# Optimization experiments

Hardware: AMD Instinct MI355X
Metric: run time of the kernel (lower is better)

Reference implementation:

```python
import jax, jax.numpy as jnp
import numpy as np

K = 8      # neighbors (from __init__ default k=8)
EPS = 1e-5 # BatchNorm1d default eps


def conv1x1(x, w, b):
    # x: (B,C,N), w: (O,C), b: (O,) -> (B,O,N)
    return jnp.einsum('bcn,oc->bon', x, w) + b[None, :, None]


def batchnorm(x, g, be):
    # training-mode BatchNorm1d: stats over (B, N) per channel
    m = x.mean(axis=(0, 2), keepdims=True)
    v = x.var(axis=(0, 2), keepdims=True)
    return g[None, :, None] * (x - m) * jax.lax.rsqrt(v + EPS) + be[None, :, None]


def block(x, w, b, g, be):
    return jax.nn.relu(batchnorm(conv1x1(x, w, b), g, be))


def setup_inputs() -> dict:
    key = jax.random.key(0)
    ks = jax.random.split(key, 24)
    B, N = 16, 4096
    rn = lambda k, s, sc=0.1: jax.random.normal(k, s, jnp.float32) * sc
    ones_n = lambda k, s: jnp.ones(s, jnp.float32) + rn(k, s, 0.01)
    return {
        'points': jax.random.normal(ks[0], (B, N, 3), jnp.float32),
        'w1': rn(ks[1], (64, 3)),   'b1': rn(ks[2], (64,)),
        'g1': ones_n(ks[3], (64,)), 'be1': rn(ks[4], (64,)),
        'w3': rn(ks[5], (512, 64)), 'b3': rn(ks[6], (512,)),
        'g3': ones_n(ks[7], (512,)), 'be3': rn(ks[8], (512,)),
        'hw1': rn(ks[9], (512, 1088)), 'hb1': rn(ks[10], (512,)),
        'hg1': ones_n(ks[11], (512,)), 'hbe1': rn(ks[12], (512,)),
        'hw2': rn(ks[13], (256, 512)), 'hb2': rn(ks[14], (256,)),
        'hg2': ones_n(ks[15], (256,)), 'hbe2': rn(ks[16], (256,)),
        'hw3': rn(ks[17], (128, 256)), 'hb3': rn(ks[18], (128,)),
        'hg3': ones_n(ks[19], (128,)), 'hbe3': rn(ks[20], (128,)),
        'hw4': rn(ks[21], (6, 128)), 'hb4': rn(ks[22], (6,)),
    }


def reference(points, w1, b1, g1, be1, w3, b3, g3, be3,
              hw1, hb1, hg1, hbe1, hw2, hb2, hg2, hbe2,
              hw3, hb3, hg3, hbe3, hw4, hb4):
    B, N, _ = points.shape
    # brute-force KNN (squared L2, ascending -> top_k on -dist)
    x2 = jnp.sum(points * points, axis=-1)                     # (B,N)
    dist = x2[:, :, None] + x2[:, None, :] \
        - 2.0 * jnp.einsum('bnd,bmd->bnm', points, points)      # (B,N,N)
    idx = jax.lax.top_k(-dist, K)[1]                           # (B,N,K) int32

    p = points.transpose(0, 2, 1)                              # (B,3,N)
    l_feat = block(p, w1, b1, g1, be1)                         # (B,64,N)
    x = block(l_feat, w3, b3, g3, be3)                         # (B,512,N)
    x_t = x.transpose(0, 2, 1)                                 # (B,N,512)

    # Faithful to the original's gather bug:
    # out[b,n,k,c] = x_t[b, idx[b,n,k], k]  (independent of c since K<512)
    vals = jnp.take_along_axis(x_t[:, :, :K], idx, axis=1)     # (B,N,K)
    m = vals.max(axis=2)                                       # (B,N)
    local_features = jnp.broadcast_to(m[:, None, :], (B, 512, N))

    global_feat = jnp.broadcast_to(x.max(axis=2, keepdims=True), (B, 512, N))
    h = jnp.concatenate([local_features, l_feat, global_feat], axis=1)  # (B,1088,N)
    h = block(h, hw1, hb1, hg1, hbe1)
    h = block(h, hw2, hb2, hg2, hbe2)
    h = block(h, hw3, hb3, hg3, hbe3)
    h = conv1x1(h, hw4, hb4)                                   # (B,6,N)
    return h.transpose(0, 2, 1)                                # (B,N,6)
```

## Files before the change

### kernel.cpp

```cpp
#include <hip/hip_runtime.h>
#include <hip/hip_bf16.h>
#include <math.h>

typedef __attribute__((ext_vector_type(8))) short short8;
typedef __attribute__((ext_vector_type(16))) float f32x16;

__device__ inline f32x16 mfma32(short8 a, short8 b, f32x16 c) {
    return __builtin_amdgcn_mfma_f32_32x32x16_bf16(a, b, c, 0, 0, 0);
}

__device__ inline void bsplit(float x, ushort& h, ushort& l) {
    __hip_bfloat16 bh = __float2bfloat16(x);
    float hf = __bfloat162float(bh);
    __hip_bfloat16 bl = __float2bfloat16(x - hf);
    h = *reinterpret_cast<ushort*>(&bh);
    l = *reinterpret_cast<ushort*>(&bl);
}

__device__ inline float unmap_f(unsigned int mp) {
    unsigned int db = mp ^ (0x80000000u | (unsigned int)((int)(~mp) >> 31));
    return __uint_as_float(db);
}

__global__ void k_wsplit_all(
    const float* __restrict__ w3s, const float* __restrict__ hw1,
    const float* __restrict__ hw2, const float* __restrict__ hw3,
    const float* __restrict__ hw4,
    ushort* __restrict__ w3h, ushort* __restrict__ w3l,
    ushort* __restrict__ w1eh, ushort* __restrict__ w1el,
    ushort* __restrict__ w2h, ushort* __restrict__ w2l,
    ushort* __restrict__ wh3h, ushort* __restrict__ wh3l,
    ushort* __restrict__ w4h, ushort* __restrict__ w4l) {
    int i = blockIdx.x * 256 + threadIdx.x;
    const float* src; int rs, co, Ms, K, base; ushort *hi, *lo;
    if (i < 32768)       { src = w3s; rs = 64;   co = 0;   Ms = 512; K = 64;  hi = w3h;  lo = w3l;  base = 0; }
    else if (i < 65536)  { src = hw1; rs = 1088; co = 512; Ms = 512; K = 64;  hi = w1eh; lo = w1el; base = 32768; }
    else if (i < 196608) { src = hw2; rs = 512;  co = 0;   Ms = 256; K = 512; hi = w2h;  lo = w2l;  base = 65536; }
    else if (i < 229376) { src = hw3; rs = 256;  co = 0;   Ms = 128; K = 256; hi = wh3h; lo = wh3l; base = 196608; }
    else if (i < 233472) { src = hw4; rs = 128;  co = 0;   Ms = 6;   K = 128; hi = w4h;  lo = w4l;  base = 229376; }
    else return;
    int li = i - base;
    int o = li / K, k = li - o * K;
    float x = (o < Ms) ? src[(size_t)o * rs + co + k] : 0.f;
    ushort h, l;
    bsplit(x, h, l);
    hi[li] = h; lo[li] = l;
}

__global__ void k_stats1(const float* __restrict__ pts, const float* __restrict__ w1,
                         const float* __restrict__ b1, float* __restrict__ part1) {
    __shared__ float sw[256];
    __shared__ float wred[2][4][64];
    int t = threadIdx.x;
    if (t < 192) sw[t] = w1[t];
    if (t < 64) sw[192 + t] = b1[t];
    __syncthreads();
    int g = blockIdx.x * 256 + t;
    float p0 = pts[g*3], p1 = pts[g*3+1], p2 = pts[g*3+2];
    int lane = t & 63, wv = t >> 6;
    for (int c = 0; c < 64; c++) {
        float y = fmaf(sw[c*3+2], p2, fmaf(sw[c*3+1], p1, fmaf(sw[c*3], p0, sw[192+c])));
        float s = y, q = y * y;
        #pragma unroll
        for (int o = 32; o > 0; o >>= 1) { s += __shfl_down(s, o); q += __shfl_down(q, o); }
        if (lane == 0) { wred[0][wv][c] = s; wred[1][wv][c] = q; }
    }
    __syncthreads();
    if (t < 64) {
        float s = wred[0][0][t] + wred[0][1][t] + wred[0][2][t] + wred[0][3][t];
        float q = wred[1][0][t] + wred[1][1][t] + wred[1][2][t] + wred[1][3][t];
        part1[blockIdx.x * 128 + t] = s;
        part1[blockIdx.x * 128 + 64 + t] = q;
    }
}

__global__ void k_fin(const float* __restrict__ part, int count, int stride, int sqoff,
                      const float* __restrict__ g, const float* __restrict__ be,
                      float* __restrict__ sout, float* __restrict__ tout) {
    int c = blockIdx.x, t = threadIdx.x;
    float s = 0.f, q = 0.f;
    for (int w = t; w < count; w += 256) { s += part[(size_t)w*stride + c]; q += part[(size_t)w*stride + sqoff + c]; }
    __shared__ float rs[4], rq[4];
    int lane = t & 63, wv = t >> 6;
    #pragma unroll
    for (int o = 32; o > 0; o >>= 1) { s += __shfl_down(s, o); q += __shfl_down(q, o); }
    if (lane == 0) { rs[wv] = s; rq[wv] = q; }
    __syncthreads();
    if (t == 0) {
        s = rs[0] + rs[1] + rs[2] + rs[3];
        q = rq[0] + rq[1] + rq[2] + rq[3];
        float mean = s / 65536.f;
        float var = q / 65536.f - mean * mean;
        float sc = g[c] * rsqrtf(var + 1e-5f);
        sout[c] = sc;
        tout[c] = be[c] - mean * sc;
    }
}

__global__ void k_lfeat2(const float* __restrict__ pts, const float* __restrict__ w1,
                         const float* __restrict__ b1, const float* __restrict__ s1,
                         const float* __restrict__ t1, ushort* __restrict__ lfh,
                         ushort* __restrict__ lfl) {
    __shared__ float sw[256], ss[64], st[64];
    int t = threadIdx.x;
    if (t < 192) sw[t] = w1[t];
    if (t < 64) { sw[192+t] = b1[t]; ss[t] = s1[t]; st[t] = t1[t]; }
    __syncthreads();
    int g = blockIdx.x * 256 + t;
    float p0 = pts[g*3], p1 = pts[g*3+1], p2 = pts[g*3+2];
    for (int c0 = 0; c0 < 64; c0 += 8) {
        union { short8 v; ushort u[8]; } H, L;
        #pragma unroll
        for (int j = 0; j < 8; j++) {
            int c = c0 + j;
            float y = fmaf(sw[c*3+2], p2, fmaf(sw[c*3+1], p1, fmaf(sw[c*3], p0, sw[192+c])));
            float a = fmaxf(fmaf(ss[c], y, st[c]), 0.f);
            bsplit(a, H.u[j], L.u[j]);
        }
        *(short8*)(lfh + (size_t)g*64 + c0) = H.v;
        *(short8*)(lfl + (size_t)g*64 + c0) = L.v;
    }
}

template<int MODE>
__global__ __launch_bounds__(256, 2) void k_gemm64(
    const ushort* __restrict__ Bhi, const ushort* __restrict__ Blo,
    const ushort* __restrict__ Ahi, const ushort* __restrict__ Alo,
    const float* __restrict__ bias, const float* __restrict__ A1,
    const float* __restrict__ G1, const float* __restrict__ mb,
    float* __restrict__ part, float* __restrict__ y38) {
    __shared__ ushort sbh[128*64], sbl[128*64];
    __shared__ float sPb[512], sPa[512];
    int t = threadIdx.x, pb = blockIdx.x;
    int gn0 = pb * 128, b = pb >> 5;
    for (int i = t; i < 512; i += 256) {
        float bb = bias[i];
        if (MODE) bb += G1[(b<<9) + i];
        sPb[i] = bb;
        sPa[i] = MODE ? A1[i] : 0.f;
    }
    for (int it = 0; it < 4; it++) {
        int s = it*256 + t;
        int n = s >> 3, c16 = s & 7;
        int off = (c16*16) ^ ((n & 7) << 4);
        int sb8 = (it*256 + (t & 192)) * 8;
        __builtin_amdgcn_global_load_lds((const char*)Bhi + (size_t)(gn0+n)*128 + off, &sbh[sb8], 16, 0, 0);
        __builtin_amdgcn_global_load_lds((const char*)Blo + (size_t)(gn0+n)*128 + off, &sbl[sb8], 16, 0, 0);
    }
    __syncthreads();
    int lane = t & 63, wv = t >> 6, m = lane & 31, kg = lane >> 5;
    for (int ct = 0; ct < 4; ct++) {
        int ch0 = wv*128 + ct*32;
        short8 ah[4], al[4];
        #pragma unroll
        for (int ks = 0; ks < 4; ks++) {
            ah[ks] = *(const short8*)(Ahi + (size_t)(ch0+m)*64 + ks*16 + kg*8);
            al[ks] = *(const short8*)(Alo + (size_t)(ch0+m)*64 + ks*16 + kg*8);
        }
        float ssum[16] = {}, ssq[16] = {}, smx[16];
        #pragma unroll
        for (int r = 0; r < 16; r++) smx[r] = -__builtin_inff();
        for (int pt = 0; pt < 4; pt++) {
            int n = pt*32 + m;
            f32x16 acc = {};
            #pragma unroll
            for (int ks = 0; ks < 4; ks++) {
                int off = ((ks*16 + kg*8)*2) ^ ((n & 7) << 4);
                short8 bh = *(const short8*)((const char*)sbh + n*128 + off);
                short8 bl = *(const short8*)((const char*)sbl + n*128 + off);
                acc = mfma32(ah[ks], bh, acc);
                acc = mfma32(ah[ks], bl, acc);
                acc = mfma32(al[ks], bh, acc);
            }
            float mval = MODE ? mb[gn0 + n] : 0.f;
            #pragma unroll
            for (int r = 0; r < 16; r++) {
                int chr = ch0 + (r&3) + 8*(r>>2) + 4*kg;
                float v = acc[r] + sPb[chr] + (MODE ? sPa[chr]*mval : 0.f);
                ssum[r] += v; ssq[r] = fmaf(v, v, ssq[r]);
                if (MODE == 0) {
                    smx[r] = fmaxf(smx[r], v);
                    if (wv == 0 && ct == 0 && r < 4) {
                        int c8 = (r&3) + 4*kg;
                        y38[(size_t)c8*65536 + gn0 + n] = v;
                    }
                }
            }
        }
        #pragma unroll
        for (int r = 0; r < 16; r++) {
            float s = ssum[r], q = ssq[r], x = smx[r];
            #pragma unroll
            for (int o = 16; o > 0; o >>= 1) {
                s += __shfl_xor(s, o); q += __shfl_xor(q, o);
                if (MODE == 0) x = fmaxf(x, __shfl_xor(x, o));
            }
            if (m == 0) {
                int chr = ch0 + (r&3) + 8*(r>>2) + 4*kg;
                if (MODE == 0) {
                    part[(size_t)pb*1536 + chr] = s;
                    part[(size_t)pb*1536 + 512 + chr] = q;
                    part[(size_t)pb*1536 + 1024 + chr] = x;
                } else {
                    part[(size_t)pb*1024 + chr] = s;
                    part[(size_t)pb*1024 + 512 + chr] = q;
                }
            }
        }
    }
}

__global__ void k_fin3b(const float* __restrict__ part3, const float* __restrict__ s3,
                        const float* __restrict__ t3, float* __restrict__ gmaxb) {
    int b = blockIdx.x, c = threadIdx.x;
    float mx = -__builtin_inff();
    for (int i = 0; i < 32; i++) mx = fmaxf(mx, part3[(size_t)(b*32+i)*1536 + 1024 + c]);
    gmaxb[(b<<9)+c] = fmaxf(fmaf(s3[c], mx, t3[c]), 0.f);
}

__global__ void k_a1g1(const float* __restrict__ hw1, const float* __restrict__ gmaxb,
                       float* __restrict__ A1, float* __restrict__ G1) {
    __shared__ float sg[512];
    int blk = blockIdx.x, t = threadIdx.x;
    if (blk < 32) {
        int b = blk >> 1;
        for (int i = t; i < 512; i += 256) sg[i] = gmaxb[(b<<9)+i];
        __syncthreads();
        int o = (blk & 1)*256 + t;
        float s = 0.f;
        for (int c4 = 0; c4 < 128; c4++) {
            float4 w = *(const float4*)&hw1[(size_t)o*1088 + 576 + c4*4];
            s = fmaf(w.x, sg[c4*4],   s);
            s = fmaf(w.y, sg[c4*4+1], s);
            s = fmaf(w.z, sg[c4*4+2], s);
            s = fmaf(w.w, sg[c4*4+3], s);
        }
        G1[(b<<9)+o] = s;
    } else {
        int o = (blk - 32)*256 + t;
        float s = 0.f;
        for (int c4 = 0; c4 < 128; c4++) {
            float4 w = *(const float4*)&hw1[(size_t)o*1088 + c4*4];
            s += w.x; s += w.y; s += w.z; s += w.w;
        }
        A1[o] = s;
    }
}

__global__ __launch_bounds__(1024, 8)
void k_knn(const float* __restrict__ pts, const float* __restrict__ y38,
           const float* __restrict__ s3, const float* __restrict__ t3,
           float* __restrict__ mbuf) {
    __shared__ float4 sp[4096];
    int t = threadIdx.x, blk = blockIdx.x;
    int b = blk >> 5;
    int lane = t & 63, wv = t >> 6;
    const float* pb = pts + (size_t)b * 4096 * 3;
    for (int i = t; i < 4096; i += 1024) {
        float c0 = pb[i*3], c1 = pb[i*3+1], c2 = pb[i*3+2];
        float cw = __fadd_rn(__fadd_rn(__fmul_rn(c0,c0), __fmul_rn(c1,c1)), __fmul_rn(c2,c2));
        sp[i] = make_float4(c0, c1, c2, cw);
    }
    __syncthreads();
    const int NINF = 0xff800000;
    int qbase = (blk & 31) * 128 + wv * 8;
    for (int pass = 0; pass < 2; ++pass) {
        int qb = qbase + pass*4;
        float q0[4], q1[4], q2[4], qx2[4];
        #pragma unroll
        for (int qi = 0; qi < 4; qi++) {
            float4 qp = sp[qb + qi];
            q0[qi] = qp.x; q1[qi] = qp.y; q2[qi] = qp.z; qx2[qi] = qp.w;
        }
        float sd[4]; unsigned int si[4]; float thr[4];
        {
            float4 cp = sp[lane];
            #pragma unroll
            for (int qi = 0; qi < 4; qi++) {
                float dot = __fadd_rn(__fadd_rn(__fmul_rn(q0[qi],cp.x), __fmul_rn(q1[qi],cp.y)), __fmul_rn(q2[qi],cp.z));
                float d = __fsub_rn(__fadd_rn(qx2[qi], cp.w), __fmul_rn(2.f, dot));
                unsigned int db = __float_as_uint(d);
                unsigned int mp = db ^ (0x80000000u | (unsigned int)((int)db >> 31));
                unsigned long long key = ((unsigned long long)mp << 32) | (unsigned int)lane;
                #pragma unroll
                for (int k = 2; k <= 64; k <<= 1) {
                    #pragma unroll
                    for (int jj = k >> 1; jj >= 1; jj >>= 1) {
                        unsigned long long pk = __shfl_xor(key, jj);
                        bool up = ((lane & k) == 0);
                        bool lower = ((lane & jj) == 0);
                        bool keepmin = (lower == up);
                        unsigned long long mn = (pk < key) ? pk : key;
                        unsigned long long mx = (pk < key) ? key : pk;
                        key = keepmin ? mn : mx;
                    }
                }
                sd[qi] = unmap_f((unsigned int)(key >> 32));
                si[qi] = (unsigned int)key;
                thr[qi] = __shfl(sd[qi], 7);
            }
        }
        for (int j = 1; j < 64; j++) {
            float4 cp = sp[j*64 + lane];
            #pragma unroll
            for (int qi = 0; qi < 4; qi++) {
                float dot = __fadd_rn(__fadd_rn(__fmul_rn(q0[qi],cp.x), __fmul_rn(q1[qi],cp.y)), __fmul_rn(q2[qi],cp.z));
                float d = __fsub_rn(__fadd_rn(qx2[qi], cp.w), __fmul_rn(2.f, dot));
                unsigned long long mask = __ballot(d < thr[qi]);
                if (mask != 0ull) {
                    do {
                        int src = __ffsll(mask) - 1;
                        float db = __uint_as_float(__builtin_amdgcn_readlane(__float_as_uint(d), src));
                        unsigned int mb_ = (unsigned int)(j*64 + src);
                        float pd = __int_as_float(__builtin_amdgcn_update_dpp(
                            NINF, __float_as_int(sd[qi]), 0x111, 0xf, 0xf, false));
                        unsigned int pi = (unsigned int)__builtin_amdgcn_update_dpp(
                            0, (int)si[qi], 0x111, 0xf, 0xf, false);
                        bool keep = (sd[qi] <= db);
                        bool pk = (pd <= db);
                        sd[qi] = keep ? sd[qi] : (pk ? db : pd);
                        si[qi] = keep ? si[qi] : (pk ? mb_ : pi);
                        mask &= (mask - 1ull);
                    } while (mask != 0ull);
                    thr[qi] = __shfl(sd[qi], 7);
                }
            }
        }
        if (lane < 8) {
            #pragma unroll
            for (int qi = 0; qi < 4; qi++) {
                float y = y38[(size_t)lane*65536 + (b<<12) + (si[qi] & 4095)];
                float mv = fmaxf(fmaf(s3[lane], y, t3[lane]), 0.f);
                mv = fmaxf(mv, __shfl_xor(mv, 1));
                mv = fmaxf(mv, __shfl_xor(mv, 2));
                mv = fmaxf(mv, __shfl_xor(mv, 4));
                if (lane == 0) mbuf[(b<<12) + qb + qi] = mv;
            }
        }
    }
}

__global__ __launch_bounds__(256, 2) void k_h2f(
    const ushort* __restrict__ lfh, const ushort* __restrict__ lfl,
    const ushort* __restrict__ W1hi, const ushort* __restrict__ W1lo,
    const ushort* __restrict__ W2hi, const ushort* __restrict__ W2lo,
    const float* __restrict__ hb1, const float* __restrict__ A1g,
    const float* __restrict__ G1g, const float* __restrict__ mb,
    const float* __restrict__ sh1, const float* __restrict__ th1,
    const float* __restrict__ hb2,
    float* __restrict__ pre2, float* __restrict__ parth2) {
    __shared__ ushort sLh[128*64], sLl[128*64];
    __shared__ ushort a1h[128*64], a1l[128*64];
    __shared__ float sP0[512], sP1[512], sSh[512];
    int t = threadIdx.x, pb = blockIdx.x;
    int gn0 = pb * 128, b = pb >> 5;
    for (int i = t; i < 512; i += 256) {
        float s = sh1[i];
        sP0[i] = fmaf(s, hb1[i] + G1g[(b<<9)+i], th1[i]);
        sP1[i] = s * A1g[i];
        sSh[i] = s;
    }
    for (int it = 0; it < 4; it++) {
        int s = it*256 + t;
        int n = s >> 3, c16 = s & 7;
        int off = (c16*16) ^ ((n & 7) << 4);
        int sb8 = (it*256 + (t & 192)) * 8;
        __builtin_amdgcn_global_load_lds((const char*)lfh + (size_t)(gn0+n)*128 + off, &sLh[sb8], 16, 0, 0);
        __builtin_amdgcn_global_load_lds((const char*)lfl + (size_t)(gn0+n)*128 + off, &sLl[sb8], 16, 0, 0);
    }
    __syncthreads();
    int lane = t & 63, wv = t >> 6, m = lane & 31, kg = lane >> 5;
    int pn = wv*32 + m;
    float mval = mb[gn0 + pn];
    f32x16 acc0[4] = {}, acc1[4] = {};
    for (int ch = 0; ch < 8; ch++) {
        #pragma unroll
        for (int cht = 0; cht < 2; cht++) {
            int cch = ch*64 + cht*32;
            f32x16 acc = {};
            #pragma unroll
            for (int ks = 0; ks < 4; ks++) {
                short8 ah = *(const short8*)(W1hi + (size_t)(cch+m)*64 + ks*16 + kg*8);
                short8 al = *(const short8*)(W1lo + (size_t)(cch+m)*64 + ks*16 + kg*8);
                int off = ((ks*16 + kg*8)*2) ^ ((m & 7) << 4);
                short8 bh = *(const short8*)((const char*)sLh + pn*128 + off);
                short8 bl = *(const short8*)((const char*)sLl + pn*128 + off);
                acc = mfma32(ah, bh, acc);
                acc = mfma32(ah, bl, acc);
                acc = mfma32(al, bh, acc);
            }
            #pragma unroll
            for (int q = 0; q < 4; q++) {
                ushort hs[4], ls[4];
                #pragma unroll
                for (int i = 0; i < 4; i++) {
                    int r = q*4 + i;
                    int chr = cch + i + 8*q + 4*kg;
                    float a = fmaxf(fmaf(sSh[chr], acc[r], sP0[chr] + sP1[chr]*mval), 0.f);
                    bsplit(a, hs[i], ls[i]);
                }
                int chb = cht*32 + 8*q + 4*kg;
                int off = (chb*2) ^ ((m & 7) << 4);
                uint2 vh, vl;
                vh.x = (uint)hs[0] | ((uint)hs[1] << 16); vh.y = (uint)hs[2] | ((uint)hs[3] << 16);
                vl.x = (uint)ls[0] | ((uint)ls[1] << 16); vl.y = (uint)ls[2] | ((uint)ls[3] << 16);
                *(uint2*)((char*)a1h + pn*128 + off) = vh;
                *(uint2*)((char*)a1l + pn*128 + off) = vl;
            }
        }
        __syncthreads();
        #pragma unroll
        for (int ks = 0; ks < 4; ks++) {
            int koc = ks*16 + kg*8;
            int kglob = ch*64 + koc;
            short8 w0h = *(const short8*)(W2hi + (size_t)(wv*64+m)*512 + kglob);
            short8 w0l = *(const short8*)(W2lo + (size_t)(wv*64+m)*512 + kglob);
            short8 w1h = *(const short8*)(W2hi + (size_t)(wv*64+32+m)*512 + kglob);
            short8 w1l = *(const short8*)(W2lo + (size_t)(wv*64+32+m)*512 + kglob);
            #pragma unroll
            for (int pt = 0; pt < 4; pt++) {
                int n = pt*32 + m;
                int off = (koc*2) ^ ((n & 7) << 4);
                short8 bh = *(const short8*)((const char*)a1h + n*128 + off);
                short8 bl = *(const short8*)((const char*)a1l + n*128 + off);
                acc0[pt] = mfma32(w0h, bh, acc0[pt]);
                acc1[pt] = mfma32(w1h, bh, acc1[pt]);
                acc0[pt] = mfma32(w0h, bl, acc0[pt]);
                acc1[pt] = mfma32(w1h, bl, acc1[pt]);
                acc0[pt] = mfma32(w0l, bh, acc0[pt]);
                acc1[pt] = mfma32(w1l, bh, acc1[pt]);
            }
        }
        __syncthreads();
    }
    #pragma unroll
    for (int ti = 0; ti < 2; ti++) {
        #pragma unroll
        for (int r = 0; r < 16; r++) {
            int chr = wv*64 + ti*32 + (r&3) + 8*(r>>2) + 4*kg;
            float hb = hb2[chr];
            float s = 0.f, q = 0.f;
            #pragma unroll
            for (int pt = 0; pt < 4; pt++) {
                float v = (ti ? acc1[pt][r] : acc0[pt][r]) + hb;
                pre2[(size_t)chr*65536 + gn0 + pt*32 + m] = v;
                s += v; q = fmaf(v, v, q);
            }
            #pragma unroll
            for (int o = 16; o > 0; o >>= 1) { s += __shfl_xor(s, o); q += __shfl_xor(q, o); }
            if (m == 0) {
                parth2[(size_t)pb*512 + chr] = s;
                parth2[(size_t)pb*512 + 256 + chr] = q;
            }
        }
    }
}

__global__ __launch_bounds__(256, 2) void k_h3s(
    const float* __restrict__ pre2, const float* __restrict__ sh2,
    const float* __restrict__ th2,
    const ushort* __restrict__ W3hi, const ushort* __restrict__ W3lo,
    const float* __restrict__ hb3, float* __restrict__ parth3,
    float* __restrict__ pre3) {
    __shared__ ushort sbh[32*256], sbl[32*256];
    __shared__ float ft[128*36];
    __shared__ float sS2[256], sT2[256];
    int t = threadIdx.x, pb = blockIdx.x;
    sS2[t] = sh2[t]; sT2[t] = th2[t];
    int lane = t & 63, wv = t >> 6, m = lane & 31, kg = lane >> 5;
    int ch0 = wv * 32;
    int cn = t & 31, cgq = t >> 5;
    float bhr[16];
    #pragma unroll
    for (int r = 0; r < 16; r++) bhr[r] = hb3[ch0 + (r&3) + 8*(r>>2) + 4*kg];
    float ssum[16] = {}, ssq[16] = {};
    for (int pt = 0; pt < 4; pt++) {
        int gn0 = pb*128 + pt*32;
        for (int h = 0; h < 2; h++) {
            __syncthreads();
            #pragma unroll
            for (int i = 0; i < 4; i++) {
                int idx = i*256 + t;
                int row = idx >> 3, c4 = idx & 7;
                float4 v = *(const float4*)(pre2 + (size_t)(h*128+row)*65536 + gn0 + c4*4);
                float* dst = &ft[row*36 + c4*4];
                dst[0] = v.x; dst[1] = v.y; dst[2] = v.z; dst[3] = v.w;
            }
            __syncthreads();
            #pragma unroll
            for (int i4 = 0; i4 < 4; i4++) {
                int cl0 = cgq*16 + i4*4;
                int cg0 = h*128 + cl0;
                ushort hs[4], ls[4];
                #pragma unroll
                for (int i = 0; i < 4; i++) {
                    float v = fmaxf(fmaf(sS2[cg0+i], ft[(cl0+i)*36 + cn], sT2[cg0+i]), 0.f);
                    bsplit(v, hs[i], ls[i]);
                }
                int off = cn*512 + (((cg0 >> 3)*16) ^ ((cn & 15) << 4)) + (cg0 & 7)*2;
                uint2 vh, vl;
                vh.x = (uint)hs[0] | ((uint)hs[1] << 16); vh.y = (uint)hs[2] | ((uint)hs[3] << 16);
                vl.x = (uint)ls[0] | ((uint)ls[1] << 16); vl.y = (uint)ls[2] | ((uint)ls[3] << 16);
                *(uint2*)((char*)sbh + off) = vh;
                *(uint2*)((char*)sbl + off) = vl;
            }
        }
        __syncthreads();
        f32x16 acc = {};
        for (int ks = 0; ks < 16; ks++) {
            int ko = ks*16 + kg*8;
            int off = (ko*2) ^ ((m & 15) << 4);
            short8 bh = *(const short8*)((const char*)sbh + m*512 + off);
            short8 bl = *(const short8*)((const char*)sbl + m*512 + off);
            short8 ah = *(const short8*)(W3hi + (size_t)(ch0+m)*256 + ko);
            short8 al = *(const short8*)(W3lo + (size_t)(ch0+m)*256 + ko);
            acc = mfma32(ah, bh, acc);
            acc = mfma32(ah, bl, acc);
            acc = mfma32(al, bh, acc);
        }
        #pragma unroll
        for (int r = 0; r < 16; r++) {
            float v = acc[r] + bhr[r];
            int chr = ch0 + (r&3) + 8*(r>>2) + 4*kg;
            pre3[(size_t)chr*65536 + gn0 + m] = v;
            ssum[r] += v; ssq[r] = fmaf(v, v, ssq[r]);
        }
    }
    #pragma unroll
    for (int r = 0; r < 16; r++) {
        float s = ssum[r], q = ssq[r];
        #pragma unroll
        for (int o = 16; o > 0; o >>= 1) { s += __shfl_xor(s, o); q += __shfl_xor(q, o); }
        if (m == 0) {
            int chr = ch0 + (r&3) + 8*(r>>2) + 4*kg;
            parth3[(size_t)pb*256 + chr] = s;
            parth3[(size_t)pb*256 + 128 + chr] = q;
        }
    }
}

__global__ __launch_bounds__(256) void k_h4l(
    const float* __restrict__ pre3, const float* __restrict__ sh3,
    const float* __restrict__ th3, const float* __restrict__ hw4,
    const float* __restrict__ hb4, float* __restrict__ out) {
    __shared__ float a3[128*66];
    __shared__ float sW[6*128];
    __shared__ float sB[8];
    int t = threadIdx.x, pb = blockIdx.x;
    int n0 = pb * 64;
    for (int i = t; i < 768; i += 256) sW[i] = hw4[i];
    if (t < 6) sB[t] = hb4[t];
    #pragma unroll
    for (int k = 0; k < 32; k++) {
        int i = k*256 + t;
        int c = i >> 6, col = i & 63;
        float v = pre3[(size_t)c*65536 + n0 + col];
        a3[c*66 + col] = fmaxf(fmaf(sh3[c], v, th3[c]), 0.f);
    }
    __syncthreads();
    int p = t & 63, grp = t >> 6;
    if (grp < 3) {
        float a0 = sB[grp*2], a1 = sB[grp*2+1];
        const float* w0 = &sW[(grp*2)*128];
        const float* w1 = &sW[(grp*2+1)*128];
        #pragma unroll 4
        for (int c = 0; c < 128; c++) {
            float x = a3[c*66 + p];
            a0 = fmaf(w0[c], x, a0);
            a1 = fmaf(w1[c], x, a1);
        }
        out[(size_t)(n0+p)*6 + grp*2]     = a0;
        out[(size_t)(n0+p)*6 + grp*2 + 1] = a1;
    }
}

extern "C" void kernel_launch(void* const* d_in, const int* in_sizes, int n_in,
                              void* d_out, int out_size, void* d_ws, size_t ws_size,
                              hipStream_t stream) {
    const float* pts  = (const float*)d_in[0];
    const float* w1   = (const float*)d_in[1];
    const float* b1   = (const float*)d_in[2];
    const float* g1   = (const float*)d_in[3];
    const float* be1  = (const float*)d_in[4];
    const float* w3   = (const float*)d_in[5];
    const float* b3   = (const float*)d_in[6];
    const float* g3   = (const float*)d_in[7];
    const float* be3  = (const float*)d_in[8];
    const float* hw1  = (const float*)d_in[9];
    const float* hb1  = (const float*)d_in[10];
    const float* hg1  = (const float*)d_in[11];
    const float* hbe1 = (const float*)d_in[12];
    const float* hw2  = (const float*)d_in[13];
    const float* hb2  = (const float*)d_in[14];
    const float* hg2  = (const float*)d_in[15];
    const float* hbe2 = (const float*)d_in[16];
    const float* hw3  = (const float*)d_in[17];
    const float* hb3  = (const float*)d_in[18];
    const float* hg3  = (const float*)d_in[19];
    const float* hbe3 = (const float*)d_in[20];
    const float* hw4  = (const float*)d_in[21];
    const float* hb4  = (const float*)d_in[22];
    (void)in_sizes; (void)n_in; (void)out_size; (void)ws_size;

    float* W = (float*)d_ws;
    size_t off = 0;
    auto alloc = [&](size_t n) { float* p = W + off; off += n; return p; };
    auto allocU = [&](size_t nshorts) { return (ushort*)alloc((nshorts + 1) / 2); };

    ushort* lfh  = allocU(65536UL*64);
    ushort* lfl  = allocU(65536UL*64);
    ushort* w3h  = allocU(512*64);  ushort* w3l  = allocU(512*64);
    ushort* w1eh = allocU(512*64);  ushort* w1el = allocU(512*64);
    ushort* w2h  = allocU(256*512); ushort* w2l  = allocU(256*512);
    ushort* wh3h = allocU(128*256); ushort* wh3l = allocU(128*256);
    ushort* w4h  = allocU(32*128);  ushort* w4l  = allocU(32*128);
    float* y38    = alloc(524288);
    float* mbuf   = alloc(65536);
    float* gmaxb  = alloc(8192);
    float* G1     = alloc(8192);
    float* A1     = alloc(512);
    float* s1 = alloc(64);  float* t1 = alloc(64);
    float* s3 = alloc(512); float* t3 = alloc(512);
    float* sh1 = alloc(512); float* th1 = alloc(512);
    float* sh2 = alloc(256); float* th2 = alloc(256);
    float* sh3 = alloc(128); float* th3 = alloc(128);
    float* part1  = alloc(32768);
    float* part3  = alloc(512*1536);
    float* parth1 = alloc(512*1024);
    float* parth2 = alloc(512*512);
    float* parth3 = alloc(512*256);
    float* pre2   = alloc(16777216);
    float* pre3   = alloc(8388608);

    k_wsplit_all<<<912, 256, 0, stream>>>(w3, hw1, hw2, hw3, hw4,
                                          w3h, w3l, w1eh, w1el, w2h, w2l,
                                          wh3h, wh3l, w4h, w4l);

    k_stats1<<<256, 256, 0, stream>>>(pts, w1, b1, part1);
    k_fin<<<64, 256, 0, stream>>>(part1, 256, 128, 64, g1, be1, s1, t1);
    k_lfeat2<<<256, 256, 0, stream>>>(pts, w1, b1, s1, t1, lfh, lfl);
    k_gemm64<0><<<512, 256, 0, stream>>>(lfh, lfl, w3h, w3l, b3, nullptr, nullptr, nullptr, part3, y38);
    k_fin<<<512, 256, 0, stream>>>(part3, 512, 1536, 512, g3, be3, s3, t3);
    k_fin3b<<<16, 512, 0, stream>>>(part3, s3, t3, gmaxb);
    k_a1g1<<<34, 256, 0, stream>>>(hw1, gmaxb, A1, G1);
    k_knn<<<512, 1024, 0, stream>>>(pts, y38, s3, t3, mbuf);
    k_gemm64<1><<<512, 256, 0, stream>>>(lfh, lfl, w1eh, w1el, hb1, A1, G1, mbuf, parth1, nullptr);
    k_fin<<<512, 256, 0, stream>>>(parth1, 512, 1024, 512, hg1, hbe1, sh1, th1);
    k_h2f<<<512, 256, 0, stream>>>(lfh, lfl, w1eh, w1el, w2h, w2l, hb1, A1, G1, mbuf,
                                   sh1, th1, hb2, pre2, parth2);
    k_fin<<<256, 256, 0, stream>>>(parth2, 512, 512, 256, hg2, hbe2, sh2, th2);
    k_h3s<<<512, 256, 0, stream>>>(pre2, sh2, th2, wh3h, wh3l, hb3, parth3, pre3);
    k_fin<<<128, 256, 0, stream>>>(parth3, 512, 256, 128, hg3, hbe3, sh3, th3);
    k_h4l<<<1024, 256, 0, stream>>>(pre3, sh3, th3, hw4, hb4, (float*)d_out);
}
```

Before: 410.2 us.

## Prune KNN search by sorting points along x and expanding a window

Adds a per-batch bitonic sort of points by x coordinate, then has the KNN kernel start each query at its sorted position and grow a 64-point window left or right until the squared x-gap exceeds the current 8th-best distance. This replaces the brute-force scan over all 4096 candidates per query, cutting distance evaluations and insertion work. Ties are broken by original index so the selected set matches top_k. It costs an extra sort kernel, serial per-query processing with data-dependent loop counts, and relies on an epsilon margin for correctness near the threshold.

Result: slower. 468.3 us (+14.2%).

```diff
diff --git a/kernel.cpp b/kernel.cpp
--- a/kernel.cpp
+++ b/kernel.cpp
@@ -247,95 +247,150 @@
     }
 }
 
+__global__ __launch_bounds__(1024) void k_sortx(
+    const float* __restrict__ pts, float4* __restrict__ sxp, int* __restrict__ sidxg) {
+    __shared__ unsigned long long key[4096];
+    int t = threadIdx.x, b = blockIdx.x;
+    const float* pb = pts + (size_t)b * 4096 * 3;
+    for (int i = t; i < 4096; i += 1024) {
+        float x = pb[i*3];
+        unsigned int xb = __float_as_uint(x);
+        unsigned int mp = xb ^ (0x80000000u | (unsigned int)((int)xb >> 31));
+        key[i] = ((unsigned long long)mp << 32) | (unsigned int)i;
+    }
+    __syncthreads();
+    for (int k = 2; k <= 4096; k <<= 1) {
+        for (int j = k >> 1; j >= 1; j >>= 1) {
+            for (int i = t; i < 4096; i += 1024) {
+                int p = i ^ j;
+                if (p > i) {
+                    bool up = ((i & k) == 0);
+                    unsigned long long a = key[i], c = key[p];
+                    if ((c < a) == up) { key[i] = c; key[p] = a; }
+                }
+            }
+            __syncthreads();
+        }
+    }
+    for (int i = t; i < 4096; i += 1024) {
+        int orig = (int)(key[i] & 0xffffffffull);
+        float c0 = pb[orig*3], c1 = pb[orig*3+1], c2 = pb[orig*3+2];
+        float cw = __fadd_rn(__fadd_rn(__fmul_rn(c0,c0), __fmul_rn(c1,c1)), __fmul_rn(c2,c2));
+        sxp[(size_t)b*4096 + i] = make_float4(c0, c1, c2, cw);
+        sidxg[(size_t)b*4096 + i] = orig;
+    }
+}
+
 __global__ __launch_bounds__(1024, 8)
-void k_knn(const float* __restrict__ pts, const float* __restrict__ y38,
+void k_knn(const float* __restrict__ pts, const float4* __restrict__ sxp,
+           const int* __restrict__ sidxg, const float* __restrict__ y38,
            const float* __restrict__ s3, const float* __restrict__ t3,
            float* __restrict__ mbuf) {
     __shared__ float4 sp[4096];
+    __shared__ int sid[4096];
     int t = threadIdx.x, blk = blockIdx.x;
     int b = blk >> 5;
     int lane = t & 63, wv = t >> 6;
-    const float* pb = pts + (size_t)b * 4096 * 3;
     for (int i = t; i < 4096; i += 1024) {
-        float c0 = pb[i*3], c1 = pb[i*3+1], c2 = pb[i*3+2];
-        float cw = __fadd_rn(__fadd_rn(__fmul_rn(c0,c0), __fmul_rn(c1,c1)), __fmul_rn(c2,c2));
-        sp[i] = make_float4(c0, c1, c2, cw);
+        sp[i] = sxp[(size_t)b*4096 + i];
+        sid[i] = sidxg[(size_t)b*4096 + i];
     }
     __syncthreads();
     const int NINF = 0xff800000;
+    const float MARG = 1e-4f;
+    const float* pq = pts + (size_t)b * 4096 * 3;
     int qbase = (blk & 31) * 128 + wv * 8;
-    for (int pass = 0; pass < 2; ++pass) {
-        int qb = qbase + pass*4;
-        float q0[4], q1[4], q2[4], qx2[4];
-        #pragma unroll
-        for (int qi = 0; qi < 4; qi++) {
-            float4 qp = sp[qb + qi];
-            q0[qi] = qp.x; q1[qi] = qp.y; q2[qi] = qp.z; qx2[qi] = qp.w;
-        }
-        float sd[4]; unsigned int si[4]; float thr[4];
+    for (int qi = 0; qi < 8; qi++) {
+        int nq = qbase + qi;
+        float q0 = pq[nq*3], q1 = pq[nq*3+1], q2 = pq[nq*3+2];
+        float qx2 = __fadd_rn(__fadd_rn(__fmul_rn(q0,q0), __fmul_rn(q1,q1)), __fmul_rn(q2,q2));
+        int cnt = (int)__popcll(__ballot(sp[lane*64].x <= q0));
+        int p0 = cnt - 1; if (p0 < 0) p0 = 0;
+        p0 *= 64;
+        float sd; unsigned int si;
         {
-            float4 cp = sp[lane];
-            #pragma unroll
-            for (int qi = 0; qi < 4; qi++) {
-                float dot = __fadd_rn(__fadd_rn(__fmul_rn(q0[qi],cp.x), __fmul_rn(q1[qi],cp.y)), __fmul_rn(q2[qi],cp.z));
-                float d = __fsub_rn(__fadd_rn(qx2[qi], cp.w), __fmul_rn(2.f, dot));
-                unsigned int db = __float_as_uint(d);
-                unsigned int mp = db ^ (0x80000000u | (unsigned int)((int)db >> 31));
-                unsigned long long key = ((unsigned long long)mp << 32) | (unsigned int)lane;
+            int ii = p0 + lane;
+            float4 cp = sp[ii];
+            int idc = sid[ii];
+            float dot = __fadd_rn(__fadd_rn(__fmul_rn(q0,cp.x), __fmul_rn(q1,cp.y)), __fmul_rn(q2,cp.z));
+            float d = __fsub_rn(__fadd_rn(qx2, cp.w), __fmul_rn(2.f, dot));
+            unsigned int db = __float_as_uint(d);
+            unsigned int mp = db ^ (0x80000000u | (unsigned int)((int)db >> 31));
+            unsigned long long key = ((unsigned long long)mp << 32) | (unsigned int)idc;
+            #pragma unroll
+            for (int k = 2; k <= 64; k <<= 1) {
                 #pragma unroll
-                for (int k = 2; k <= 64; k <<= 1) {
-                    #pragma unroll
-                    for (int jj = k >> 1; jj >= 1; jj >>= 1) {
-                        unsigned long long pk = __shfl_xor(key, jj);
-                        bool up = ((lane & k) == 0);
-                        bool lower = ((lane & jj) == 0);
-                        bool keepmin = (lower == up);
-                        unsigned long long mn = (pk < key) ? pk : key;
-                        unsigned long long mx = (pk < key) ? key : pk;
-                        key = keepmin ? mn : mx;
-                    }
+                for (int jj = k >> 1; jj >= 1; jj >>= 1) {
+                    unsigned long long pk = __shfl_xor(key, jj);
+                    bool up = ((lane & k) == 0);
+                    bool lower = ((lane & jj) == 0);
+                    bool keepmin = (lower == up);
+                    unsigned long long mn = (pk < key) ? pk : key;
+                    unsigned long long mx = (pk < key) ? key : pk;
+                    key = keepmin ? mn : mx;
                 }
-                sd[qi] = unmap_f((unsigned int)(key >> 32));
-                si[qi] = (unsigned int)key;
-                thr[qi] = __shfl(sd[qi], 7);
-            }
-        }
-        for (int j = 1; j < 64; j++) {
-            float4 cp = sp[j*64 + lane];
-            #pragma unroll
-            for (int qi = 0; qi < 4; qi++) {
-                float dot = __fadd_rn(__fadd_rn(__fmul_rn(q0[qi],cp.x), __fmul_rn(q1[qi],cp.y)), __fmul_rn(q2[qi],cp.z));
-                float d = __fsub_rn(__fadd_rn(qx2[qi], cp.w), __fmul_rn(2.f, dot));
-                unsigned long long mask = __ballot(d < thr[qi]);
-                if (mask != 0ull) {
-                    do {
-                        int src = __ffsll(mask) - 1;
-                        float db = __uint_as_float(__builtin_amdgcn_readlane(__float_as_uint(d), src));
-                        unsigned int mb_ = (unsigned int)(j*64 + src);
-                        float pd = __int_as_float(__builtin_amdgcn_update_dpp(
-                            NINF, __float_as_int(sd[qi]), 0x111, 0xf, 0xf, false));
-                        unsigned int pi = (unsigned int)__builtin_amdgcn_update_dpp(
-                            0, (int)si[qi], 0x111, 0xf, 0xf, false);
-                        bool keep = (sd[qi] <= db);
-                        bool pk = (pd <= db);
-                        sd[qi] = keep ? sd[qi] : (pk ? db : pd);
-                        si[qi] = keep ? si[qi] : (pk ? mb_ : pi);
-                        mask &= (mask - 1ull);
-                    } while (mask != 0ull);
-                    thr[qi] = __shfl(sd[qi], 7);
-                }
+            }
+            sd = unmap_f((unsigned int)(key >> 32));
+            si = (unsigned int)key;
+        }
+        float thr = __shfl(sd, 7);
+        unsigned int thri = __shfl(si, 7);
+        int wlo = p0, whi = p0 + 64;
+        while (true) {
+            bool aliveL = (wlo > 0);
+            float bl2 = 0.f;
+            if (aliveL) {
+                float dl = __fsub_rn(q0, sp[wlo-1].x);
+                bl2 = __fmul_rn(dl, dl);
+                aliveL = (bl2 <= thr + MARG);
+            }
+            bool aliveR = (whi < 4096);
+            float br2 = 0.f;
+            if (aliveR) {
+                float dr = __fsub_rn(sp[whi].x, q0);
+                br2 = __fmul_rn(dr, dr);
+                aliveR = (br2 <= thr + MARG);
+            }
+            if (!aliveL && !aliveR) break;
+            bool goL = aliveL && (!aliveR || bl2 <= br2);
+            int base;
+            if (goL) { base = wlo - 64; wlo = (base < 0) ? 0 : base; }
+            else     { base = whi; whi = (whi + 64 > 4096) ? 4096 : whi + 64; }
+            int ii = base + lane;
+            bool valid = (ii >= 0) && (ii < 4096);
+            int ic = valid ? ii : p0;
+            float4 cp = sp[ic];
+            int idc = sid[ic];
+            float dot = __fadd_rn(__fadd_rn(__fmul_rn(q0,cp.x), __fmul_rn(q1,cp.y)), __fmul_rn(q2,cp.z));
+            float d = __fsub_rn(__fadd_rn(qx2, cp.w), __fmul_rn(2.f, dot));
+            if (!valid) d = __builtin_inff();
+            unsigned long long mask = __ballot(d < thr || (d == thr && (unsigned int)idc < thri));
+            if (mask != 0ull) {
+                do {
+                    int src = __ffsll(mask) - 1;
+                    float db = __uint_as_float(__builtin_amdgcn_readlane(__float_as_uint(d), src));
+                    unsigned int idb = (unsigned int)__builtin_amdgcn_readlane(idc, src);
+                    float pd = __int_as_float(__builtin_amdgcn_update_dpp(
+                        NINF, __float_as_int(sd), 0x111, 0xf, 0xf, false));
+                    unsigned int pi = (unsigned int)__builtin_amdgcn_update_dpp(
+                        0, (int)si, 0x111, 0xf, 0xf, false);
+                    bool keep = (sd < db) || (sd == db && si < idb);
+                    bool pk   = (pd < db) || (pd == db && pi < idb);
+                    sd = keep ? sd : (pk ? db : pd);
+                    si = keep ? si : (pk ? idb : pi);
+                    mask &= (mask - 1ull);
+                } while (mask != 0ull);
+                thr = __shfl(sd, 7);
+                thri = __shfl(si, 7);
             }
         }
         if (lane < 8) {
-            #pragma unroll
-            for (int qi = 0; qi < 4; qi++) {
-                float y = y38[(size_t)lane*65536 + (b<<12) + (si[qi] & 4095)];
-                float mv = fmaxf(fmaf(s3[lane], y, t3[lane]), 0.f);
-                mv = fmaxf(mv, __shfl_xor(mv, 1));
-                mv = fmaxf(mv, __shfl_xor(mv, 2));
-                mv = fmaxf(mv, __shfl_xor(mv, 4));
-                if (lane == 0) mbuf[(b<<12) + qb + qi] = mv;
-            }
+            float y = y38[(size_t)lane*65536 + (b<<12) + (si & 4095)];
+            float mv = fmaxf(fmaf(s3[lane], y, t3[lane]), 0.f);
+            mv = fmaxf(mv, __shfl_xor(mv, 1));
+            mv = fmaxf(mv, __shfl_xor(mv, 2));
+            mv = fmaxf(mv, __shfl_xor(mv, 4));
+            if (lane == 0) mbuf[(b<<12) + nq] = mv;
         }
     }
 }
@@ -631,10 +686,13 @@
     float* parth3 = alloc(512*256);
     float* pre2   = alloc(16777216);
     float* pre3   = alloc(8388608);
+    float4* sxp   = (float4*)alloc(65536UL*4);
+    int* sidxg    = (int*)alloc(65536);
 
     k_wsplit_all<<<912, 256, 0, stream>>>(w3, hw1, hw2, hw3, hw4,
                                           w3h, w3l, w1eh, w1el, w2h, w2l,
                                           wh3h, wh3l, w4h, w4l);
+    k_sortx<<<16, 1024, 0, stream>>>(pts, sxp, sidxg);
 
     k_stats1<<<256, 256, 0, stream>>>(pts, w1, b1, part1);
     k_fin<<<64, 256, 0, stream>>>(part1, 256, 128, 64, g1, be1, s1, t1);
@@ -643,7 +701,7 @@
     k_fin<<<512, 256, 0, stream>>>(part3, 512, 1536, 512, g3, be3, s3, t3);
     k_fin3b<<<16, 512, 0, stream>>>(part3, s3, t3, gmaxb);
     k_a1g1<<<34, 256, 0, stream>>>(hw1, gmaxb, A1, G1);
-    k_knn<<<512, 1024, 0, stream>>>(pts, y38, s3, t3, mbuf);
+    k_knn<<<512, 1024, 0, stream>>>(pts, sxp, sidxg, y38, s3, t3, mbuf);
     k_gemm64<1><<<512, 256, 0, stream>>>(lfh, lfl, w1eh, w1el, hb1, A1, G1, mbuf, parth1, nullptr);
     k_fin<<<512, 256, 0, stream>>>(parth1, 512, 1024, 512, hg1, hbe1, sh1, th1);
     k_h2f<<<512, 256, 0, stream>>>(lfh, lfl, w1eh, w1el, w2h, w2l, hb1, A1, G1, mbuf,
```

## Sort points by x and prune KNN search with expanding window

Applied to the files above, without the earlier changes.

Adds a per-batch bitonic sort of points by x coordinate, then rewrites the KNN kernel to start from each query's neighbourhood in sorted order and expand left or right in 64-point chunks. Expansion stops once the squared x-gap exceeds the current 8th-best distance plus a small margin, skipping most of the brute-force N² distance scan. Ties are broken by original index so the selected set matches the reference ordering. This costs an extra sort kernel and the buffers for sorted points, and pruning efficiency depends on the point distribution.

Result: slower. 475.0 us (+15.8%).

```diff
diff --git a/kernel.cpp b/kernel.cpp
--- a/kernel.cpp
+++ b/kernel.cpp
@@ -247,41 +247,77 @@
     }
 }
 
+__global__ __launch_bounds__(1024) void k_sortx(
+    const float* __restrict__ pts, float4* __restrict__ sxp, int* __restrict__ sidxg) {
+    __shared__ unsigned long long key[4096];
+    int t = threadIdx.x, b = blockIdx.x;
+    const float* pb = pts + (size_t)b * 4096 * 3;
+    for (int i = t; i < 4096; i += 1024) {
+        float x = pb[i*3];
+        unsigned int xb = __float_as_uint(x);
+        unsigned int mp = xb ^ (0x80000000u | (unsigned int)((int)xb >> 31));
+        key[i] = ((unsigned long long)mp << 32) | (unsigned int)i;
+    }
+    __syncthreads();
+    for (int k = 2; k <= 4096; k <<= 1) {
+        for (int j = k >> 1; j >= 1; j >>= 1) {
+            #pragma unroll 2
+            for (int q = t; q < 2048; q += 1024) {
+                int i = ((q & ~(j-1)) << 1) | (q & (j-1));
+                int p = i | j;
+                bool up = ((i & k) == 0);
+                unsigned long long a = key[i], c = key[p];
+                if ((c < a) == up) { key[i] = c; key[p] = a; }
+            }
+            __syncthreads();
+        }
+    }
+    for (int i = t; i < 4096; i += 1024) {
+        int orig = (int)(key[i] & 0xffffffffull);
+        float c0 = pb[orig*3], c1 = pb[orig*3+1], c2 = pb[orig*3+2];
+        float cw = __fadd_rn(__fadd_rn(__fmul_rn(c0,c0), __fmul_rn(c1,c1)), __fmul_rn(c2,c2));
+        sxp[(size_t)b*4096 + i] = make_float4(c0, c1, c2, cw);
+        sidxg[(size_t)b*4096 + i] = orig;
+    }
+}
+
 __global__ __launch_bounds__(1024, 8)
-void k_knn(const float* __restrict__ pts, const float* __restrict__ y38,
-           const float* __restrict__ s3, const float* __restrict__ t3,
-           float* __restrict__ mbuf) {
+void k_knn(const float4* __restrict__ sxp, const int* __restrict__ sidxg,
+           const float* __restrict__ y38, const float* __restrict__ s3,
+           const float* __restrict__ t3, float* __restrict__ mbuf) {
     __shared__ float4 sp[4096];
+    __shared__ int sid[4096];
     int t = threadIdx.x, blk = blockIdx.x;
     int b = blk >> 5;
     int lane = t & 63, wv = t >> 6;
-    const float* pb = pts + (size_t)b * 4096 * 3;
     for (int i = t; i < 4096; i += 1024) {
-        float c0 = pb[i*3], c1 = pb[i*3+1], c2 = pb[i*3+2];
-        float cw = __fadd_rn(__fadd_rn(__fmul_rn(c0,c0), __fmul_rn(c1,c1)), __fmul_rn(c2,c2));
-        sp[i] = make_float4(c0, c1, c2, cw);
+        sp[i] = sxp[(size_t)b*4096 + i];
+        sid[i] = sidxg[(size_t)b*4096 + i];
     }
     __syncthreads();
     const int NINF = 0xff800000;
-    int qbase = (blk & 31) * 128 + wv * 8;
+    const float MARG = 1e-4f;
     for (int pass = 0; pass < 2; ++pass) {
-        int qb = qbase + pass*4;
-        float q0[4], q1[4], q2[4], qx2[4];
+        int qbase = (blk & 31) * 128 + pass*64 + wv*4;
+        float q0[4], q1[4], q2[4], qx2[4]; int qid[4];
         #pragma unroll
         for (int qi = 0; qi < 4; qi++) {
-            float4 qp = sp[qb + qi];
+            float4 qp = sp[qbase + qi];
             q0[qi] = qp.x; q1[qi] = qp.y; q2[qi] = qp.z; qx2[qi] = qp.w;
-        }
-        float sd[4]; unsigned int si[4]; float thr[4];
+            qid[qi] = sid[qbase + qi];
+        }
+        int wlo = qbase & ~63, whi = (qbase & ~63) + 64;
+        float sd[4]; unsigned int si[4]; float thr[4]; unsigned int thri[4];
         {
-            float4 cp = sp[lane];
+            float4 cp = sp[wlo + lane];
+            int idc = sid[wlo + lane];
             #pragma unroll
             for (int qi = 0; qi < 4; qi++) {
                 float dot = __fadd_rn(__fadd_rn(__fmul_rn(q0[qi],cp.x), __fmul_rn(q1[qi],cp.y)), __fmul_rn(q2[qi],cp.z));
                 float d = __fsub_rn(__fadd_rn(qx2[qi], cp.w), __fmul_rn(2.f, dot));
                 unsigned int db = __float_as_uint(d);
                 unsigned int mp = db ^ (0x80000000u | (unsigned int)((int)db >> 31));
-                unsigned long long key = ((unsigned long long)mp << 32) | (unsigned int)lane;
+                unsigned long long key = ((unsigned long long)mp << 32) | (unsigned int)idc;
                 #pragma unroll
                 for (int k = 2; k <= 64; k <<= 1) {
                     #pragma unroll
@@ -298,31 +334,71 @@
                 sd[qi] = unmap_f((unsigned int)(key >> 32));
                 si[qi] = (unsigned int)key;
                 thr[qi] = __shfl(sd[qi], 7);
-            }
-        }
-        for (int j = 1; j < 64; j++) {
-            float4 cp = sp[j*64 + lane];
+                thri[qi] = __shfl(si[qi], 7);
+            }
+        }
+        while (true) {
+            bool aliveL = (wlo > 0);
+            float blm = __builtin_inff();
+            if (aliveL) {
+                float xb = sp[wlo-1].x;
+                bool any = false;
+                #pragma unroll
+                for (int qi = 0; qi < 4; qi++) {
+                    float dl = __fsub_rn(q0[qi], xb);
+                    float d2 = __fmul_rn(dl, dl);
+                    if (d2 <= thr[qi] + MARG) any = true;
+                    blm = fminf(blm, d2);
+                }
+                aliveL = any;
+            }
+            bool aliveR = (whi < 4096);
+            float brm = __builtin_inff();
+            if (aliveR) {
+                float xb = sp[whi].x;
+                bool any = false;
+                #pragma unroll
+                for (int qi = 0; qi < 4; qi++) {
+                    float dr = __fsub_rn(xb, q0[qi]);
+                    float d2 = __fmul_rn(dr, dr);
+                    if (d2 <= thr[qi] + MARG) any = true;
+                    brm = fminf(brm, d2);
+                }
+                aliveR = any;
+            }
+            if (!aliveL && !aliveR) break;
+            bool goL = aliveL && (!aliveR || blm <= brm);
+            int base;
+            if (goL) { base = wlo - 64; wlo = (base < 0) ? 0 : base; }
+            else     { base = whi; whi = (whi + 64 > 4096) ? 4096 : whi + 64; }
+            int ii = base + lane;
+            bool valid = (ii >= 0) && (ii < 4096);
+            int ic = valid ? ii : 0;
+            float4 cp = sp[ic];
+            int idc = sid[ic];
             #pragma unroll
             for (int qi = 0; qi < 4; qi++) {
                 float dot = __fadd_rn(__fadd_rn(__fmul_rn(q0[qi],cp.x), __fmul_rn(q1[qi],cp.y)), __fmul_rn(q2[qi],cp.z));
                 float d = __fsub_rn(__fadd_rn(qx2[qi], cp.w), __fmul_rn(2.f, dot));
-                unsigned long long mask = __ballot(d < thr[qi]);
+                if (!valid) d = __builtin_inff();
+                unsigned long long mask = __ballot(d < thr[qi] || (d == thr[qi] && (unsigned int)idc < thri[qi]));
                 if (mask != 0ull) {
                     do {
                         int src = __ffsll(mask) - 1;
                         float db = __uint_as_float(__builtin_amdgcn_readlane(__float_as_uint(d), src));
-                        unsigned int mb_ = (unsigned int)(j*64 + src);
+                        unsigned int idb = (unsigned int)__builtin_amdgcn_readlane(idc, src);
                         float pd = __int_as_float(__builtin_amdgcn_update_dpp(
                             NINF, __float_as_int(sd[qi]), 0x111, 0xf, 0xf, false));
                         unsigned int pi = (unsigned int)__builtin_amdgcn_update_dpp(
                             0, (int)si[qi], 0x111, 0xf, 0xf, false);
-                        bool keep = (sd[qi] <= db);
-                        bool pk = (pd <= db);
+                        bool keep = (sd[qi] < db) || (sd[qi] == db && si[qi] < idb);
+                        bool pk   = (pd < db) || (pd == db && pi < idb);
                         sd[qi] = keep ? sd[qi] : (pk ? db : pd);
-                        si[qi] = keep ? si[qi] : (pk ? mb_ : pi);
+                        si[qi] = keep ? si[qi] : (pk ? idb : pi);
                         mask &= (mask - 1ull);
                     } while (mask != 0ull);
                     thr[qi] = __shfl(sd[qi], 7);
+                    thri[qi] = __shfl(si[qi], 7);
                 }
             }
         }
@@ -334,7 +410,7 @@
                 mv = fmaxf(mv, __shfl_xor(mv, 1));
                 mv = fmaxf(mv, __shfl_xor(mv, 2));
                 mv = fmaxf(mv, __shfl_xor(mv, 4));
-                if (lane == 0) mbuf[(b<<12) + qb + qi] = mv;
+                if (lane == 0) mbuf[(b<<12) + qid[qi]] = mv;
             }
         }
     }
@@ -631,10 +707,13 @@
     float* parth3 = alloc(512*256);
     float* pre2   = alloc(16777216);
     float* pre3   = alloc(8388608);
+    float4* sxp   = (float4*)alloc(65536UL*4);
+    int* sidxg    = (int*)alloc(65536);
 
     k_wsplit_all<<<912, 256, 0, stream>>>(w3, hw1, hw2, hw3, hw4,
                                           w3h, w3l, w1eh, w1el, w2h, w2l,
                                           wh3h, wh3l, w4h, w4l);
+    k_sortx<<<16, 1024, 0, stream>>>(pts, sxp, sidxg);
 
     k_stats1<<<256, 256, 0, stream>>>(pts, w1, b1, part1);
     k_fin<<<64, 256, 0, stream>>>(part1, 256, 128, 64, g1, be1, s1, t1);
@@ -643,7 +722,7 @@
     k_fin<<<512, 256, 0, stream>>>(part3, 512, 1536, 512, g3, be3, s3, t3);
     k_fin3b<<<16, 512, 0, stream>>>(part3, s3, t3, gmaxb);
     k_a1g1<<<34, 256, 0, stream>>>(hw1, gmaxb, A1, G1);
-    k_knn<<<512, 1024, 0, stream>>>(pts, y38, s3, t3, mbuf);
+    k_knn<<<512, 1024, 0, stream>>>(sxp, sidxg, y38, s3, t3, mbuf);
     k_gemm64<1><<<512, 256, 0, stream>>>(lfh, lfl, w1eh, w1el, hb1, A1, G1, mbuf, parth1, nullptr);
     k_fin<<<512, 256, 0, stream>>>(parth1, 512, 1024, 512, hg1, hbe1, sh1, th1);
     k_h2f<<<512, 256, 0, stream>>>(lfh, lfl, w1eh, w1el, w2h, w2l, hb1, A1, G1, mbuf,
```
